# Kernel optimization log

Measured on AMD Instinct MI355X. Metric: run time of the kernel, lower is better.

Reference implementation:

```python
import jax, jax.numpy as jnp
import numpy as np

N = 50000        # nodes
E_RND = 800000   # random directed edges (avg degree 16)
B = 4            # batch
D_IN = 64
D_OUT = 64


def setup_inputs() -> dict:
    key = jax.random.key(0)
    k1, k2, k3, k4 = jax.random.split(key, 4)
    self_loops = jnp.arange(N, dtype=jnp.int32)
    # edge list of A_tilde = A + I  (random A, plus self-loops)
    rows = jnp.concatenate([jax.random.randint(k1, (E_RND,), 0, N, dtype=jnp.int32), self_loops])
    cols = jnp.concatenate([jax.random.randint(k2, (E_RND,), 0, N, dtype=jnp.int32), self_loops])
    # deg = row sums of A_tilde; A_hat[i,j] = A_tilde[i,j] / sqrt(deg[i]*deg[j])
    deg = jax.ops.segment_sum(jnp.ones(rows.shape[0], jnp.float32), rows, num_segments=N)
    deg = jnp.maximum(deg, 1.0)
    a_vals = 1.0 / jnp.sqrt(deg[rows] * deg[cols])
    x = jax.random.normal(k3, (B, N, D_IN), dtype=jnp.float32)
    # he_uniform-like scale for the dense kernel
    W = jax.random.uniform(k4, (D_IN, D_OUT), dtype=jnp.float32,
                           minval=-1.0, maxval=1.0) * np.float32(np.sqrt(6.0 / D_IN))
    return {"x": x, "W": W, "rows": rows, "cols": cols, "a_vals": a_vals}


def reference(x, W, rows, cols, a_vals):
    """GCN layer: out[b] = (A_hat @ x[b]) @ W, A_hat given as COO edge list."""
    n = x.shape[1]

    def spmm(xb):  # xb: [N, D_in]
        msgs = xb[cols] * a_vals[:, None]          # [E, D_in]
        return jax.ops.segment_sum(msgs, rows, num_segments=n)  # [N, D_in]

    y = jax.vmap(spmm)(x)                          # [B, N, D_in]
    return jnp.einsum('bnd,do->bno', y, W)         # [B, N, D_out]
```

## Files before the change

### kernel.cpp

```cpp
#include <hip/hip_runtime.h>

#define D 64
#define PACK 256

typedef __attribute__((ext_vector_type(8))) short bf16x8;
typedef __attribute__((ext_vector_type(4))) float f32x4;

__device__ __forceinline__ unsigned short f2bf(float f) {
  unsigned int u = __float_as_uint(f);
  u += 0x7FFFu + ((u >> 16) & 1u);
  return (unsigned short)(u >> 16);
}
__device__ __forceinline__ float bf2f(unsigned short h) {
  union { unsigned int u; float f; } v;
  v.u = ((unsigned int)h) << 16;
  return v.f;
}

__global__ __launch_bounds__(256) void gemm_hist_kernel(
    const float* __restrict__ x, const float* __restrict__ W,
    unsigned short* __restrict__ xwb, const int* __restrict__ rows,
    int* __restrict__ cnt, int total_nodes, int N, int E) {
  const int tid  = threadIdx.x;
  const int lane = tid & 63;
  const int c = lane & 15;
  const int q = lane >> 4;

  bf16x8 Bf[4][2];
#pragma unroll
  for (int nt = 0; nt < 4; ++nt) {
#pragma unroll
    for (int h = 0; h < 2; ++h) {
      const int n  = nt * 16 + c;
      const int k0 = h * 32 + q * 8;
#pragma unroll
      for (int j = 0; j < 8; ++j)
        Bf[nt][h][j] = (short)f2bf(W[(k0 + j) * D + n]);
    }
  }

  const float4* __restrict__ x4 = (const float4*)x;
  const int ntiles = (total_nodes + 15) >> 4;
  const int wave_g = blockIdx.x * 4 + (tid >> 6);
  const int nwaves = gridDim.x * 4;

  for (int tile = wave_g; tile < ntiles; tile += nwaves) {
    const int base = tile * 16;
    const int node = min(base + c, total_nodes - 1);
    const float4* xr = x4 + (size_t)node * 16;
    const float4 p0 = xr[q * 2 + 0];
    const float4 p1 = xr[q * 2 + 1];
    const float4 p2 = xr[8 + q * 2 + 0];
    const float4 p3 = xr[8 + q * 2 + 1];
    bf16x8 a0, a1;
    a0[0] = (short)f2bf(p0.x); a0[1] = (short)f2bf(p0.y);
    a0[2] = (short)f2bf(p0.z); a0[3] = (short)f2bf(p0.w);
    a0[4] = (short)f2bf(p1.x); a0[5] = (short)f2bf(p1.y);
    a0[6] = (short)f2bf(p1.z); a0[7] = (short)f2bf(p1.w);
    a1[0] = (short)f2bf(p2.x); a1[1] = (short)f2bf(p2.y);
    a1[2] = (short)f2bf(p2.z); a1[3] = (short)f2bf(p2.w);
    a1[4] = (short)f2bf(p3.x); a1[5] = (short)f2bf(p3.y);
    a1[6] = (short)f2bf(p3.z); a1[7] = (short)f2bf(p3.w);

    f32x4 acc[4];
#pragma unroll
    for (int nt = 0; nt < 4; ++nt) {
      f32x4 z = {0.f, 0.f, 0.f, 0.f};
      z = __builtin_amdgcn_mfma_f32_16x16x32_bf16(a0, Bf[nt][0], z, 0, 0, 0);
      z = __builtin_amdgcn_mfma_f32_16x16x32_bf16(a1, Bf[nt][1], z, 0, 0, 0);
      acc[nt] = z;
    }
#pragma unroll
    for (int r = 0; r < 4; ++r) {
      const int fn = base + q * 4 + r;
      if (fn >= total_nodes) break;
      const int b  = (fn >= N) + (fn >= 2 * N) + (fn >= 3 * N);
      const int nn = fn - b * N;
      unsigned short* dst = xwb + (size_t)nn * PACK + b * D + c;
#pragma unroll
      for (int nt = 0; nt < 4; ++nt) dst[nt * 16] = f2bf(acc[nt][r]);
    }
  }

  const int gtid = blockIdx.x * 256 + tid;
  const int gstr = gridDim.x * 256;
  for (int e = gtid; e < E; e += gstr) atomicAdd(&cnt[rows[e]], 1);
}

__global__ __launch_bounds__(1024) void scan_a_kernel(
    const int* __restrict__ cnt, int* __restrict__ start,
    int* __restrict__ partial, int n) {
  __shared__ int s[1024];
  const int t = threadIdx.x;
  const int i = blockIdx.x * 1024 + t;
  const int v = (i < n) ? cnt[i] : 0;
  s[t] = v;
  __syncthreads();
  for (int off = 1; off < 1024; off <<= 1) {
    const int u = (t >= off) ? s[t - off] : 0;
    __syncthreads();
    s[t] += u;
    __syncthreads();
  }
  if (i < n) start[i] = s[t] - v;
  if (t == 1023) partial[blockIdx.x] = s[1023];
}

__global__ __launch_bounds__(1024) void scan_bc_kernel(
    const int* __restrict__ partial, int* __restrict__ start,
    int* __restrict__ cursor, int n, int E) {
  __shared__ int soff;
  if (threadIdx.x < 64) {
    int v = 0;
    for (int j = threadIdx.x; j < (int)blockIdx.x; j += 64) v += partial[j];
#pragma unroll
    for (int d = 32; d > 0; d >>= 1) v += __shfl_down(v, d);
    if (threadIdx.x == 0) soff = v;
  }
  __syncthreads();
  const int i = blockIdx.x * 1024 + threadIdx.x;
  if (i < n) {
    const int sv = start[i] + soff;
    start[i] = sv;
    cursor[i] = sv;
  }
  if (blockIdx.x == 0 && threadIdx.x == 0) start[n] = E;
}

__global__ __launch_bounds__(256) void permute_kernel(
    const int* __restrict__ rows, const int* __restrict__ cols,
    const float* __restrict__ a_vals, int* __restrict__ cursor,
    int2* __restrict__ meta, int E) {
  const int e = blockIdx.x * blockDim.x + threadIdx.x;
  if (e >= E) return;
  const int pos = atomicAdd(&cursor[rows[e]], 1);
  meta[pos] = make_int2(cols[e], __float_as_int(a_vals[e]));
}

__global__ __launch_bounds__(256) void gather_kernel(
    const unsigned short* __restrict__ xwb, const int* __restrict__ start,
    const int2* __restrict__ meta, float* __restrict__ out,
    int N, int stride_b) {
  const int lane = threadIdx.x & 63;
  const int r = blockIdx.x * 4 + (threadIdx.x >> 6);
  if (r >= N) return;

  int j0 = start[r];
  const int je = start[r + 1];
  const ushort4* __restrict__ xw4 = (const ushort4*)xwb;

  float ax = 0.f, ay = 0.f, az = 0.f, aw = 0.f;
  while (j0 < je) {
    const int cnt = min(64, je - j0);
    const int2 mv = meta[j0 + min(lane, cnt - 1)];
#pragma unroll
    for (int k = 0; k < 64; k += 8) {
      if (k >= cnt) break;
      int   cc[8];
      float aa[8];
      ushort4 uu[8];
#pragma unroll
      for (int i = 0; i < 8; ++i) {
        cc[i] = __builtin_amdgcn_readlane(mv.x, k + i);
        aa[i] = (k + i < cnt)
                    ? __int_as_float(__builtin_amdgcn_readlane(mv.y, k + i))
                    : 0.f;
      }
#pragma unroll
      for (int i = 0; i < 8; ++i)
        uu[i] = xw4[(size_t)cc[i] * 64 + lane];
#pragma unroll
      for (int i = 0; i < 8; ++i) {
        ax = fmaf(aa[i], bf2f(uu[i].x), ax);
        ay = fmaf(aa[i], bf2f(uu[i].y), ay);
        az = fmaf(aa[i], bf2f(uu[i].z), az);
        aw = fmaf(aa[i], bf2f(uu[i].w), aw);
      }
    }
    j0 += 64;
  }

  const int i0 = lane * 4;
  const int b  = i0 >> 6;
  const int ch = i0 & 63;
  float4 o;
  o.x = ax; o.y = ay; o.z = az; o.w = aw;
  *(float4*)(out + (size_t)b * stride_b + (size_t)r * D + ch) = o;
}

extern "C" void kernel_launch(void* const* d_in, const int* in_sizes, int n_in,
                              void* d_out, int out_size, void* d_ws,
                              size_t ws_size, hipStream_t stream) {
  const float* x      = (const float*)d_in[0];
  const float* W      = (const float*)d_in[1];
  const int*   rows   = (const int*)d_in[2];
  const int*   cols   = (const int*)d_in[3];
  const float* a_vals = (const float*)d_in[4];

  const int E           = in_sizes[2];
  const int total_nodes = in_sizes[0] / D;
  const int N           = total_nodes / 4;
  const int stride_b    = N * D;

  char* ws = (char*)d_ws;
  unsigned short* xwb = (unsigned short*)ws;  ws += (size_t)N * PACK * sizeof(unsigned short);
  int2* meta   = (int2*)ws;                   ws += (size_t)E * sizeof(int2);
  int* start   = (int*)ws;                    ws += (size_t)(N + 4) * sizeof(int);
  int* cursor  = (int*)ws;                    ws += (size_t)N * sizeof(int);
  int* partial = (int*)ws;

  hipMemsetAsync(cursor, 0, (size_t)N * sizeof(int), stream);

  gemm_hist_kernel<<<2048, 256, 0, stream>>>(x, W, xwb, rows, cursor,
                                             total_nodes, N, E);

  const int sb = (N + 1023) / 1024;
  scan_a_kernel<<<sb, 1024, 0, stream>>>(cursor, start, partial, N);
  scan_bc_kernel<<<sb, 1024, 0, stream>>>(partial, start, cursor, N, E);

  const int eb = (E + 255) / 256;
  permute_kernel<<<eb, 256, 0, stream>>>(rows, cols, a_vals, cursor, meta, E);

  const int gb = (N + 3) / 4;
  gather_kernel<<<gb, 256, 0, stream>>>(xwb, start, meta, (float*)d_out, N,
                                        stride_b);
}
```

Baseline: 252.2 us.

## Split gather wave into half-waves loading two edges with 16-byte reads

The gather kernel now has each half of a wave process a different edge. Each lane loads 8 bf16 values (16 bytes) instead of 4, and the two halves' partial sums are combined with a cross-lane shuffle. The kernel also becomes a persistent grid-stride loop over rows with a fixed grid of 2048 blocks instead of one wave per row. The aim is fewer, wider memory requests per edge and more loads in flight, at the cost of an extra shuffle reduction and more registers per lane.

```diff
diff --git a/kernel.cpp b/kernel.cpp
--- a/kernel.cpp
+++ b/kernel.cpp
@@ -5,6 +5,7 @@
 
 typedef __attribute__((ext_vector_type(8))) short bf16x8;
 typedef __attribute__((ext_vector_type(4))) float f32x4;
+typedef __attribute__((ext_vector_type(8))) unsigned short ushort8;
 
 __device__ __forceinline__ unsigned short f2bf(float f) {
   unsigned int u = __float_as_uint(f);
@@ -142,50 +143,58 @@
     const int2* __restrict__ meta, float* __restrict__ out,
     int N, int stride_b) {
   const int lane = threadIdx.x & 63;
-  const int r = blockIdx.x * 4 + (threadIdx.x >> 6);
-  if (r >= N) return;
-
-  int j0 = start[r];
-  const int je = start[r + 1];
-  const ushort4* __restrict__ xw4 = (const ushort4*)xwb;
-
-  float ax = 0.f, ay = 0.f, az = 0.f, aw = 0.f;
-  while (j0 < je) {
-    const int cnt = min(64, je - j0);
-    const int2 mv = meta[j0 + min(lane, cnt - 1)];
-#pragma unroll
-    for (int k = 0; k < 64; k += 8) {
-      if (k >= cnt) break;
-      int   cc[8];
-      float aa[8];
-      ushort4 uu[8];
-#pragma unroll
-      for (int i = 0; i < 8; ++i) {
-        cc[i] = __builtin_amdgcn_readlane(mv.x, k + i);
-        aa[i] = (k + i < cnt)
-                    ? __int_as_float(__builtin_amdgcn_readlane(mv.y, k + i))
-                    : 0.f;
+  const int h = lane >> 5;
+  const int c = lane & 31;
+  const int wid = blockIdx.x * 4 + (threadIdx.x >> 6);
+  const int nw = gridDim.x * 4;
+  const ushort8* __restrict__ xw8 = (const ushort8*)xwb;
+
+  for (int r = wid; r < N; r += nw) {
+    int j0 = start[r];
+    const int je = start[r + 1];
+
+    float acc[8] = {0.f, 0.f, 0.f, 0.f, 0.f, 0.f, 0.f, 0.f};
+    while (j0 < je) {
+      const int cnt = min(64, je - j0);
+      const int2 mv = meta[j0 + min(lane, cnt - 1)];
+#pragma unroll
+      for (int k = 0; k < 64; k += 16) {
+        if (k >= cnt) break;
+        ushort8 uu[8];
+        float aa[8];
+#pragma unroll
+        for (int i = 0; i < 8; ++i) {
+          const int s0 = k + 2 * i;
+          const int c0 = __builtin_amdgcn_readlane(mv.x, s0);
+          const int c1 = __builtin_amdgcn_readlane(mv.x, s0 + 1);
+          const int a0 = __builtin_amdgcn_readlane(mv.y, s0);
+          const int a1 = __builtin_amdgcn_readlane(mv.y, s0 + 1);
+          const int cc = h ? c1 : c0;
+          const float av = __int_as_float(h ? a1 : a0);
+          aa[i] = (s0 + h < cnt) ? av : 0.f;
+          uu[i] = xw8[(size_t)cc * 32 + c];
+        }
+#pragma unroll
+        for (int i = 0; i < 8; ++i) {
+#pragma unroll
+          for (int j = 0; j < 8; ++j)
+            acc[j] = fmaf(aa[i], bf2f(uu[i][j]), acc[j]);
+        }
       }
-#pragma unroll
-      for (int i = 0; i < 8; ++i)
-        uu[i] = xw4[(size_t)cc[i] * 64 + lane];
-#pragma unroll
-      for (int i = 0; i < 8; ++i) {
-        ax = fmaf(aa[i], bf2f(uu[i].x), ax);
-        ay = fmaf(aa[i], bf2f(uu[i].y), ay);
-        az = fmaf(aa[i], bf2f(uu[i].z), az);
-        aw = fmaf(aa[i], bf2f(uu[i].w), aw);
-      }
-    }
-    j0 += 64;
-  }
-
-  const int i0 = lane * 4;
-  const int b  = i0 >> 6;
-  const int ch = i0 & 63;
-  float4 o;
-  o.x = ax; o.y = ay; o.z = az; o.w = aw;
-  *(float4*)(out + (size_t)b * stride_b + (size_t)r * D + ch) = o;
+      j0 += 64;
+    }
+
+#pragma unroll
+    for (int j = 0; j < 8; ++j) acc[j] += __shfl_xor(acc[j], 32);
+
+    const int i0 = c * 8 + h * 4;
+    const int b  = i0 >> 6;
+    const int ch = i0 & 63;
+    float4 o;
+    o.x = acc[h * 4 + 0]; o.y = acc[h * 4 + 1];
+    o.z = acc[h * 4 + 2]; o.w = acc[h * 4 + 3];
+    *(float4*)(out + (size_t)b * stride_b + (size_t)r * D + ch) = o;
+  }
 }
 
 extern "C" void kernel_launch(void* const* d_in, const int* in_sizes, int n_in,
@@ -221,7 +230,6 @@
   const int eb = (E + 255) / 256;
   permute_kernel<<<eb, 256, 0, stream>>>(rows, cols, a_vals, cursor, meta, E);
 
-  const int gb = (N + 3) / 4;
-  gather_kernel<<<gb, 256, 0, stream>>>(xwb, start, meta, (float*)d_out, N,
-                                        stride_b);
-}
+  gather_kernel<<<2048, 256, 0, stream>>>(xwb, start, meta, (float*)d_out, N,
+                                          stride_b);
+}
```

Result: no change. 254.7 us (+1.0%).
